# Kernel tuning notes

Measured on AMD Instinct MI355X. Metric: run time of the kernel, lower is better.

Reference implementation:

```python
import jax, jax.numpy as jnp
import numpy as np

B, S, D, H = 2, 2048, 1024, 16
HD = D // H  # 64


def setup_inputs() -> dict:
    key = jax.random.key(0)
    ks = jax.random.split(key, 12)
    scale = 1.0 / np.sqrt(D)
    inp = {
        "input_query": jax.random.normal(ks[0], (B, S, D), jnp.float32),
        "input_key": jax.random.normal(ks[1], (B, S, D), jnp.float32),
        "input_value": jax.random.normal(ks[2], (B, S, D), jnp.float32),
        "mask": jax.random.randint(ks[3], (B, 1, S), 0, 2, jnp.int32),
        # torch nn.Linear params: y = x @ W.T + b, W shape (out, in)
        "wq": jax.random.uniform(ks[4], (D, D), jnp.float32, -scale, scale),
        "bq": jax.random.uniform(ks[5], (D,), jnp.float32, -scale, scale),
        "wk": jax.random.uniform(ks[6], (D, D), jnp.float32, -scale, scale),
        "bk": jax.random.uniform(ks[7], (D,), jnp.float32, -scale, scale),
        "wv": jax.random.uniform(ks[8], (D, D), jnp.float32, -scale, scale),
        "bv": jax.random.uniform(ks[9], (D,), jnp.float32, -scale, scale),
        "wo": jax.random.uniform(ks[10], (D, D), jnp.float32, -scale, scale),
        "bo": jax.random.uniform(ks[11], (D,), jnp.float32, -scale, scale),
    }
    return inp


def _split_heads(x):
    # (B, S, D) -> (B, H, S, HD)
    return x.reshape(B, S, H, HD).transpose(0, 2, 1, 3)


def reference(input_query, input_key, input_value, mask, wq, bq, wk, bk, wv, bv, wo, bo):
    q = _split_heads(input_query @ wq.T + bq)
    k = _split_heads(input_key @ wk.T + bk)
    v = _split_heads(input_value @ wv.T + bv)

    # scaled dot-product attention (materializes [B,H,S,S] as the original does)
    scores = jnp.einsum("bhqd,bhkd->bhqk", q, k) / np.sqrt(HD).astype(np.float32)
    # mask: (B, 1, S) -> unsqueeze(1) -> (B, 1, 1, S); fill -1e9 where mask == 0
    m = mask[:, None, :, :]
    scores = jnp.where(m == 0, jnp.float32(-1e9), scores)
    p_attn = jax.nn.softmax(scores, axis=-1)  # dropout is identity (rate 0 / eval)

    out = jnp.einsum("bhqk,bhkd->bhqd", p_attn, v)
    out = out.transpose(0, 2, 1, 3).reshape(B, S, D)
    return out @ wo.T + bo
```

## Files before the change

kernel.cpp:

```cpp
#include <hip/hip_runtime.h>
#include <math.h>

#define BB 2
#define SS 2048
#define DD 1024
#define HH 16
#define HD 64

typedef short short8 __attribute__((ext_vector_type(8)));
typedef float floatx4 __attribute__((ext_vector_type(4)));
typedef float floatx16 __attribute__((ext_vector_type(16)));
typedef unsigned int uintx2 __attribute__((ext_vector_type(2)));

__device__ inline ushort f2bf_rne(float x) {
    union { float f; unsigned u; } v; v.f = x;
    unsigned r = v.u + 0x7FFFu + ((v.u >> 16) & 1u);
    return (ushort)(r >> 16);
}
__device__ inline float bf2f(ushort h) {
    union { unsigned u; float f; } v; v.u = ((unsigned)h) << 16;
    return v.f;
}
__device__ inline unsigned cvt_pk_bf16(float lo, float hi) {
    unsigned r;
    asm("v_cvt_pk_bf16_f32 %0, %1, %2" : "=v"(r) : "v"(lo), "v"(hi));
    return r;
}
__device__ inline short8 mk_pf(uintx2 x, uintx2 y) {
    union { unsigned u[4]; short8 s; } t;
    t.u[0] = x[0]; t.u[1] = y[0]; t.u[2] = x[1]; t.u[3] = y[1];
    return t.s;
}

__global__ __launch_bounds__(256)
void convert_bf16(const float* __restrict__ xq, const float* __restrict__ xk,
                  const float* __restrict__ xv,
                  const float* __restrict__ wq, const float* __restrict__ wk,
                  const float* __restrict__ wv, const float* __restrict__ wo,
                  ushort* __restrict__ Xq, ushort* __restrict__ Xk,
                  ushort* __restrict__ Xv,
                  ushort* __restrict__ Wq, ushort* __restrict__ Wk,
                  ushort* __restrict__ Wv, ushort* __restrict__ Wo)
{
    const int z = blockIdx.z;
    const size_t i = ((size_t)blockIdx.x * 256 + threadIdx.x) * 8;

    const float* src;
    ushort* dst;
    size_t off;
    if (z < 3) {
        src = (z == 0) ? xq : (z == 1) ? xk : xv;
        dst = (z == 0) ? Xq : (z == 1) ? Xk : Xv;
        off = i;
    } else {
        const int seg = (int)(i >> 20);
        off = i & ((1u << 20) - 1);
        src = (seg == 0) ? wq : (seg == 1) ? wk : (seg == 2) ? wv : wo;
        dst = (seg == 0) ? Wq : (seg == 1) ? Wk : (seg == 2) ? Wv : Wo;
    }
    float x[8];
    *(float4*)&x[0] = *(const float4*)(src + off);
    *(float4*)&x[4] = *(const float4*)(src + off + 4);
    short8 h8;
#pragma unroll
    for (int j = 0; j < 8; ++j) h8[j] = (short)f2bf_rne(x[j]);
    *(short8*)&dst[off] = h8;
}

#define LDK 40

__global__ __launch_bounds__(256, 3)
void qkv_gemm(const ushort* __restrict__ Xq, const ushort* __restrict__ Xk,
              const ushort* __restrict__ Xv,
              const ushort* __restrict__ Wq, const ushort* __restrict__ Wk,
              const ushort* __restrict__ Wv,
              const float* __restrict__ bq, const float* __restrict__ bk,
              const float* __restrict__ bv, const int* __restrict__ mask,
              ushort* __restrict__ Qo, ushort* __restrict__ Ko,
              ushort* __restrict__ Vo, float qscale)
{
    __shared__ ushort Alds[128][LDK];
    __shared__ ushort Blds[128][LDK];

    const int z   = blockIdx.z;
    const int tid = threadIdx.x;

    const ushort* X    = (z == 0) ? Xq : (z == 1) ? Xk : Xv;
    const ushort* W    = (z == 0) ? Wq : (z == 1) ? Wk : Wv;
    const float*  bias = (z == 0) ? bq : (z == 1) ? bk : bv;
    const float   osc  = (z == 0) ? qscale : 1.0f;

    const int lane = tid & 63;
    const int wave = tid >> 6;
    const int wr = wave >> 1;
    const int wc = wave & 1;
    const int lt = lane & 15;
    const int lq = lane >> 4;
    const int m0 = blockIdx.y * 128;
    const int n0 = blockIdx.x * 128;

    floatx4 acc[4][4];
#pragma unroll
    for (int mi = 0; mi < 4; ++mi)
#pragma unroll
        for (int ni = 0; ni < 4; ++ni) acc[mi][ni] = (floatx4)0.0f;

    const int srow = tid >> 1;
    const int sks  = (tid & 1) << 4;
    const size_t xrow = (size_t)(m0 + srow) * DD;
    const size_t wrow = (size_t)(n0 + srow) * DD;

    for (int k0 = 0; k0 < DD; k0 += 32) {
        const short8 a0 = *(const short8*)(X + xrow + k0 + sks);
        const short8 a1 = *(const short8*)(X + xrow + k0 + sks + 8);
        const short8 b0 = *(const short8*)(W + wrow + k0 + sks);
        const short8 b1 = *(const short8*)(W + wrow + k0 + sks + 8);

        __syncthreads();
        *(short8*)&Alds[srow][sks]     = a0;
        *(short8*)&Alds[srow][sks + 8] = a1;
        *(short8*)&Blds[srow][sks]     = b0;
        *(short8*)&Blds[srow][sks + 8] = b1;
        __syncthreads();

        short8 af[4], bf_[4];
#pragma unroll
        for (int mi = 0; mi < 4; ++mi)
            af[mi] = *(const short8*)&Alds[wr * 64 + mi * 16 + lt][lq * 8];
#pragma unroll
        for (int ni = 0; ni < 4; ++ni)
            bf_[ni] = *(const short8*)&Blds[wc * 64 + ni * 16 + lt][lq * 8];

#pragma unroll
        for (int mi = 0; mi < 4; ++mi)
#pragma unroll
            for (int ni = 0; ni < 4; ++ni)
                acc[mi][ni] = __builtin_amdgcn_mfma_f32_16x16x32_bf16(af[mi], bf_[ni], acc[mi][ni], 0, 0, 0);
    }

    float bbv[4];
#pragma unroll
    for (int ni = 0; ni < 4; ++ni) bbv[ni] = bias[n0 + wc * 64 + ni * 16 + lt];

    if (z <= 1) {
        ushort* C = z ? Ko : Qo;
#pragma unroll
        for (int mi = 0; mi < 4; ++mi)
#pragma unroll
            for (int ni = 0; ni < 4; ++ni) {
                const int n = n0 + wc * 64 + ni * 16 + lt;
                const int h = n >> 6;
#pragma unroll
                for (int r = 0; r < 4; ++r) {
                    const int m = m0 + wr * 64 + mi * 16 + lq * 4 + r;
                    const int b = m >> 11;
                    const int s = m & (SS - 1);
                    C[(size_t)((b * HH + h) * SS + s) * HD + (n & 63)] =
                        f2bf_rne((acc[mi][ni][r] + bbv[ni]) * osc);
                }
            }
    } else {
#pragma unroll
        for (int mi = 0; mi < 4; ++mi) {
            const int mb  = m0 + wr * 64 + mi * 16 + lq * 4;
            const int bb_ = mb >> 11;
            const int s   = mb & (SS - 1);
            const int4 mm = *(const int4*)(mask + bb_ * SS + s);
            const float mf0 = (float)mm.x, mf1 = (float)mm.y;
            const float mf2 = (float)mm.z, mf3 = (float)mm.w;
#pragma unroll
            for (int ni = 0; ni < 4; ++ni) {
                const int n = n0 + wc * 64 + ni * 16 + lt;
                const int h = n >> 6;
                ushort4 pack;
                pack.x = f2bf_rne((acc[mi][ni][0] + bbv[ni]) * mf0);
                pack.y = f2bf_rne((acc[mi][ni][1] + bbv[ni]) * mf1);
                pack.z = f2bf_rne((acc[mi][ni][2] + bbv[ni]) * mf2);
                pack.w = f2bf_rne((acc[mi][ni][3] + bbv[ni]) * mf3);
                *(ushort4*)&Vo[(size_t)((bb_ * HH + h) * HD + (n & 63)) * SS + s] = pack;
            }
        }
    }
}

#define ATQ 128
#define LDV 68

__global__ __launch_bounds__(256, 2)
void attn_mfma(const ushort* __restrict__ Qb, const ushort* __restrict__ Kb,
               const ushort* __restrict__ Vt, const int* __restrict__ mask,
               ushort* __restrict__ Ob)
{
    __shared__ __align__(16) ushort Klds[2][64][LDV];
    __shared__ __align__(16) ushort Vlds[2][64][LDV];
    __shared__ __align__(16) ushort Mlds[SS];

    const int tid  = threadIdx.x;
    const int lane = tid & 63;
    const int wave = tid >> 6;
    const int ll   = lane & 31;
    const int hi   = lane >> 5;

    const int bid    = blockIdx.x;
    const int xcd    = bid & 7;
    const int slot   = bid >> 3;
    const int bhloc  = slot >> 4;
    const int qi     = slot & 15;
    const int bh     = xcd * 4 + bhloc;
    const int b      = bh >> 4;
    const int q0     = qi * ATQ;

    const size_t sbase = (size_t)bh * SS * HD;
    const size_t vbase = (size_t)bh * HD * SS;

    {
        const int4 m0 = *(const int4*)(mask + b * SS + tid * 8);
        const int4 m1 = *(const int4*)(mask + b * SS + tid * 8 + 4);
        short8 mv;
        mv[0] = m0.x ? (short)0x3F80 : (short)0;
        mv[1] = m0.y ? (short)0x3F80 : (short)0;
        mv[2] = m0.z ? (short)0x3F80 : (short)0;
        mv[3] = m0.w ? (short)0x3F80 : (short)0;
        mv[4] = m1.x ? (short)0x3F80 : (short)0;
        mv[5] = m1.y ? (short)0x3F80 : (short)0;
        mv[6] = m1.z ? (short)0x3F80 : (short)0;
        mv[7] = m1.w ? (short)0x3F80 : (short)0;
        *(short8*)&Mlds[tid * 8] = mv;
    }

    short8 qf[4];
    const size_t qrow = sbase + (size_t)(q0 + wave * 32 + ll) * HD;
#pragma unroll
    for (int dc = 0; dc < 4; ++dc)
        qf[dc] = *(const short8*)(Qb + qrow + dc * 16 + hi * 8);

    floatx16 oacc[2];
    oacc[0] = (floatx16)0.0f;
    oacc[1] = (floatx16)0.0f;
    floatx16 lacc = (floatx16)0.0f;

    const int srow = tid >> 2;
    const int sp8  = (tid & 3) << 4;

    short8 kr0, kr1, vr0, vr1;

    {
        const size_t koff = sbase + (size_t)srow * HD + sp8;
        kr0 = *(const short8*)(Kb + koff);
        kr1 = *(const short8*)(Kb + koff + 8);
        const size_t voff = vbase + (size_t)srow * SS + sp8;
        vr0 = *(const short8*)(Vt + voff);
        vr1 = *(const short8*)(Vt + voff + 8);
        *(short8*)&Klds[0][srow][sp8]     = kr0;
        *(short8*)&Klds[0][srow][sp8 + 8] = kr1;
        *(short8*)&Vlds[0][srow][sp8]     = vr0;
        *(short8*)&Vlds[0][srow][sp8 + 8] = vr1;
    }

    const int NT = SS / 64;
    for (int kt = 0; kt < NT; ++kt) {
        const int cur = kt & 1;
        __syncthreads();

        if (kt + 1 < NT) {
            const int k0n = (kt + 1) * 64;
            const size_t koff = sbase + (size_t)(k0n + srow) * HD + sp8;
            kr0 = *(const short8*)(Kb + koff);
            kr1 = *(const short8*)(Kb + koff + 8);
            const size_t voff = vbase + (size_t)srow * SS + k0n + sp8;
            vr0 = *(const short8*)(Vt + voff);
            vr1 = *(const short8*)(Vt + voff + 8);
        }

#pragma unroll
        for (int sub = 0; sub < 2; ++sub) {
            floatx16 sacc = (floatx16)0.0f;
#pragma unroll
            for (int dc = 0; dc < 4; ++dc) {
                const short8 kf = *(const short8*)&Klds[cur][sub * 32 + ll][dc * 16 + hi * 8];
                sacc = __builtin_amdgcn_mfma_f32_32x32x16_bf16(kf, qf[dc], sacc, 0, 0, 0);
            }

            float p[16];
#pragma unroll
            for (int r = 0; r < 16; ++r) p[r] = exp2f(sacc[r]);

            const unsigned pk_a = cvt_pk_bf16(p[0],  p[1]);
            const unsigned pk_b = cvt_pk_bf16(p[2],  p[3]);
            const unsigned pk_c = cvt_pk_bf16(p[4],  p[5]);
            const unsigned pk_d = cvt_pk_bf16(p[6],  p[7]);
            const unsigned pk_e = cvt_pk_bf16(p[8],  p[9]);
            const unsigned pk_f = cvt_pk_bf16(p[10], p[11]);
            const unsigned pk_g = cvt_pk_bf16(p[12], p[13]);
            const unsigned pk_h = cvt_pk_bf16(p[14], p[15]);
            const uintx2 s1 = __builtin_amdgcn_permlane32_swap(pk_a, pk_c, false, false);
            const uintx2 s2 = __builtin_amdgcn_permlane32_swap(pk_b, pk_d, false, false);
            const uintx2 s3 = __builtin_amdgcn_permlane32_swap(pk_e, pk_g, false, false);
            const uintx2 s4 = __builtin_amdgcn_permlane32_swap(pk_f, pk_h, false, false);
            const short8 pf0 = mk_pf(s1, s2);
            const short8 pf1 = mk_pf(s3, s4);

            const int kbase = kt * 64 + sub * 32;
            const short8 mf0 = *(const short8*)&Mlds[kbase + hi * 8];
            const short8 mf1 = *(const short8*)&Mlds[kbase + 16 + hi * 8];
            lacc = __builtin_amdgcn_mfma_f32_32x32x16_bf16(pf0, mf0, lacc, 0, 0, 0);
            lacc = __builtin_amdgcn_mfma_f32_32x32x16_bf16(pf1, mf1, lacc, 0, 0, 0);

#pragma unroll
            for (int dn = 0; dn < 2; ++dn) {
                const short8 vf0 = *(const short8*)&Vlds[cur][dn * 32 + ll][sub * 32 + hi * 8];
                const short8 vf1 = *(const short8*)&Vlds[cur][dn * 32 + ll][sub * 32 + 16 + hi * 8];
                oacc[dn] = __builtin_amdgcn_mfma_f32_32x32x16_bf16(pf0, vf0, oacc[dn], 0, 0, 0);
                oacc[dn] = __builtin_amdgcn_mfma_f32_32x32x16_bf16(pf1, vf1, oacc[dn], 0, 0, 0);
            }
        }

        if (kt + 1 < NT) {
            const int nxt = cur ^ 1;
            *(short8*)&Klds[nxt][srow][sp8]     = kr0;
            *(short8*)&Klds[nxt][srow][sp8 + 8] = kr1;
            *(short8*)&Vlds[nxt][srow][sp8]     = vr0;
            *(short8*)&Vlds[nxt][srow][sp8 + 8] = vr1;
        }
    }

    const int h = bh & 15;
    float linv[16];
#pragma unroll
    for (int r = 0; r < 16; ++r) linv[r] = 1.0f / lacc[r];
#pragma unroll
    for (int dn = 0; dn < 2; ++dn)
#pragma unroll
        for (int r = 0; r < 16; ++r) {
            const int q = q0 + wave * 32 + (r & 3) + 8 * (r >> 2) + 4 * hi;
            Ob[(size_t)(b * SS + q) * DD + h * HD + dn * 32 + ll] =
                f2bf_rne(oacc[dn][r] * linv[r]);
        }
}

__global__ __launch_bounds__(256, 3)
void o_gemm(const ushort* __restrict__ A, const ushort* __restrict__ B,
            const float* __restrict__ bias, float* __restrict__ out)
{
    __shared__ ushort sA[128][LDK];
    __shared__ ushort sB[64][LDK];

    const int tid  = threadIdx.x;
    const int lane = tid & 63;
    const int wave = tid >> 6;
    const int wr = wave >> 1;
    const int wc = wave & 1;
    const int lt = lane & 15;
    const int lq = lane >> 4;
    const int m0 = blockIdx.y * 128;
    const int n0 = blockIdx.x * 64;

    floatx4 acc[4][2];
#pragma unroll
    for (int mi = 0; mi < 4; ++mi)
#pragma unroll
        for (int ni = 0; ni < 2; ++ni) acc[mi][ni] = (floatx4)0.0f;

    const int arow = tid >> 1, apart = (tid & 1) << 4;
    const int brow = tid >> 2, bpart = (tid & 3) << 3;

    for (int k0 = 0; k0 < DD; k0 += 32) {
        const size_t aoff = (size_t)(m0 + arow) * DD + k0 + apart;
        const size_t boff = (size_t)(n0 + brow) * DD + k0 + bpart;
        const short8 a0 = *(const short8*)(A + aoff);
        const short8 a1 = *(const short8*)(A + aoff + 8);
        const short8 b0 = *(const short8*)(B + boff);

        __syncthreads();
        *(short8*)&sA[arow][apart]     = a0;
        *(short8*)&sA[arow][apart + 8] = a1;
        *(short8*)&sB[brow][bpart]     = b0;
        __syncthreads();

        short8 af[4], bf_[2];
#pragma unroll
        for (int mi = 0; mi < 4; ++mi)
            af[mi] = *(const short8*)&sA[wr * 64 + mi * 16 + lt][lq * 8];
#pragma unroll
        for (int ni = 0; ni < 2; ++ni)
            bf_[ni] = *(const short8*)&sB[wc * 32 + ni * 16 + lt][lq * 8];

#pragma unroll
        for (int mi = 0; mi < 4; ++mi)
#pragma unroll
            for (int ni = 0; ni < 2; ++ni)
                acc[mi][ni] = __builtin_amdgcn_mfma_f32_16x16x32_bf16(af[mi], bf_[ni], acc[mi][ni], 0, 0, 0);
    }

#pragma unroll
    for (int mi = 0; mi < 4; ++mi)
#pragma unroll
        for (int ni = 0; ni < 2; ++ni) {
            const int n = n0 + wc * 32 + ni * 16 + lt;
            const float bb = bias[n];
#pragma unroll
            for (int r = 0; r < 4; ++r) {
                const int m = m0 + wr * 64 + mi * 16 + lq * 4 + r;
                out[(size_t)m * DD + n] = acc[mi][ni][r] + bb;
            }
        }
}

extern "C" void kernel_launch(void* const* d_in, const int* in_sizes, int n_in,
                              void* d_out, int out_size, void* d_ws, size_t ws_size,
                              hipStream_t stream) {
    const float* xq   = (const float*)d_in[0];
    const float* xk   = (const float*)d_in[1];
    const float* xv   = (const float*)d_in[2];
    const int*   mask = (const int*)d_in[3];
    const float* wq   = (const float*)d_in[4];
    const float* bq   = (const float*)d_in[5];
    const float* wk   = (const float*)d_in[6];
    const float* bk   = (const float*)d_in[7];
    const float* wv   = (const float*)d_in[8];
    const float* bv   = (const float*)d_in[9];
    const float* wo   = (const float*)d_in[10];
    const float* bo   = (const float*)d_in[11];
    float* out = (float*)d_out;

    const size_t n = (size_t)BB * SS * DD;
    const size_t w1 = (size_t)DD * DD;

    ushort* Xqb = (ushort*)d_ws;
    ushort* Xkb = Xqb + n;
    ushort* Xvb = Xkb + n;
    ushort* Kb  = Xvb + n;
    ushort* Vt  = Kb + n;
    ushort* Wob = Vt + n;
    ushort* Ob  = Xqb;

    ushort* Qb  = (ushort*)out;
    ushort* Wqb = Qb + n;
    ushort* Wkb = Wqb + w1;
    ushort* Wvb = Wkb + w1;

    const float qscale = 0.125f * 1.44269504088896340736f;

    dim3 gc(2048, 1, 4);
    convert_bf16<<<gc, 256, 0, stream>>>(xq, xk, xv, wq, wk, wv, wo,
                                         Xqb, Xkb, Xvb, Wqb, Wkb, Wvb, Wob);

    dim3 g1(DD / 128, (BB * SS) / 128, 3);
    qkv_gemm<<<g1, 256, 0, stream>>>(Xqb, Xkb, Xvb, Wqb, Wkb, Wvb,
                                     bq, bk, bv, mask, Qb, Kb, Vt, qscale);

    attn_mfma<<<dim3(512), 256, 0, stream>>>(Qb, Kb, Vt, mask, Ob);

    dim3 g2(DD / 64, (BB * SS) / 128);
    o_gemm<<<g2, 256, 0, stream>>>(Ob, Wob, bo, out);
}
```

Measured before the change: 238.4 us.

## Split attention waves over query pairs and key halves, fold mask into K

The mask is now applied by zeroing masked K rows during the K projection. Masked keys then give a score of zero, so exp2 of them is 1. The row-sum denominator subtracts the count of masked keys, which removes the per-tile mask LDS reads and lets the row sum use a constant ones operand. Each attention wave now handles two 32-row query groups over half of each 64-key tile, so every K fragment read from LDS is reused across two query groups. The two key halves are then combined through shared memory at the end. This adds register pressure, an LDS reduction epilogue and extra syncs, and it relies on masked scores without max-subtraction staying numerically safe.

New measurement: 241.0 us. About the same (+1.1%).

```diff
diff --git a/kernel.cpp b/kernel.cpp
--- a/kernel.cpp
+++ b/kernel.cpp
@@ -142,24 +142,7 @@
 #pragma unroll
     for (int ni = 0; ni < 4; ++ni) bbv[ni] = bias[n0 + wc * 64 + ni * 16 + lt];
 
-    if (z <= 1) {
-        ushort* C = z ? Ko : Qo;
-#pragma unroll
-        for (int mi = 0; mi < 4; ++mi)
-#pragma unroll
-            for (int ni = 0; ni < 4; ++ni) {
-                const int n = n0 + wc * 64 + ni * 16 + lt;
-                const int h = n >> 6;
-#pragma unroll
-                for (int r = 0; r < 4; ++r) {
-                    const int m = m0 + wr * 64 + mi * 16 + lq * 4 + r;
-                    const int b = m >> 11;
-                    const int s = m & (SS - 1);
-                    C[(size_t)((b * HH + h) * SS + s) * HD + (n & 63)] =
-                        f2bf_rne((acc[mi][ni][r] + bbv[ni]) * osc);
-                }
-            }
-    } else {
+    if (z == 2) {
 #pragma unroll
         for (int mi = 0; mi < 4; ++mi) {
             const int mb  = m0 + wr * 64 + mi * 16 + lq * 4;
@@ -180,6 +163,30 @@
                 *(ushort4*)&Vo[(size_t)((bb_ * HH + h) * HD + (n & 63)) * SS + s] = pack;
             }
         }
+    } else {
+        ushort* C = z ? Ko : Qo;
+#pragma unroll
+        for (int mi = 0; mi < 4; ++mi) {
+            const int mb  = m0 + wr * 64 + mi * 16 + lq * 4;
+            const int bb_ = mb >> 11;
+            const int s   = mb & (SS - 1);
+            float mf[4] = {1.0f, 1.0f, 1.0f, 1.0f};
+            if (z == 1) {
+                const int4 mm = *(const int4*)(mask + bb_ * SS + s);
+                mf[0] = (float)mm.x; mf[1] = (float)mm.y;
+                mf[2] = (float)mm.z; mf[3] = (float)mm.w;
+            }
+#pragma unroll
+            for (int ni = 0; ni < 4; ++ni) {
+                const int n = n0 + wc * 64 + ni * 16 + lt;
+                const int h = n >> 6;
+#pragma unroll
+                for (int r = 0; r < 4; ++r) {
+                    C[(size_t)((bb_ * HH + h) * SS + (s + r)) * HD + (n & 63)] =
+                        f2bf_rne((acc[mi][ni][r] + bbv[ni]) * osc * mf[r]);
+                }
+            }
+        }
     }
 }
 
@@ -193,13 +200,17 @@
 {
     __shared__ __align__(16) ushort Klds[2][64][LDV];
     __shared__ __align__(16) ushort Vlds[2][64][LDV];
-    __shared__ __align__(16) ushort Mlds[SS];
+    __shared__ float CmbO[2][2][16][64];
+    __shared__ float CmbL[2][16][64];
+    __shared__ int   Wsum[4];
 
     const int tid  = threadIdx.x;
     const int lane = tid & 63;
     const int wave = tid >> 6;
     const int ll   = lane & 31;
     const int hi   = lane >> 5;
+    const int qh   = wave & 1;
+    const int ks   = wave >> 1;
 
     const int bid    = blockIdx.x;
     const int xcd    = bid & 7;
@@ -214,30 +225,35 @@
     const size_t vbase = (size_t)bh * HD * SS;
 
     {
-        const int4 m0 = *(const int4*)(mask + b * SS + tid * 8);
-        const int4 m1 = *(const int4*)(mask + b * SS + tid * 8 + 4);
-        short8 mv;
-        mv[0] = m0.x ? (short)0x3F80 : (short)0;
-        mv[1] = m0.y ? (short)0x3F80 : (short)0;
-        mv[2] = m0.z ? (short)0x3F80 : (short)0;
-        mv[3] = m0.w ? (short)0x3F80 : (short)0;
-        mv[4] = m1.x ? (short)0x3F80 : (short)0;
-        mv[5] = m1.y ? (short)0x3F80 : (short)0;
-        mv[6] = m1.z ? (short)0x3F80 : (short)0;
-        mv[7] = m1.w ? (short)0x3F80 : (short)0;
-        *(short8*)&Mlds[tid * 8] = mv;
-    }
-
-    short8 qf[4];
-    const size_t qrow = sbase + (size_t)(q0 + wave * 32 + ll) * HD;
-#pragma unroll
-    for (int dc = 0; dc < 4; ++dc)
-        qf[dc] = *(const short8*)(Qb + qrow + dc * 16 + hi * 8);
-
-    floatx16 oacc[2];
-    oacc[0] = (floatx16)0.0f;
-    oacc[1] = (floatx16)0.0f;
-    floatx16 lacc = (floatx16)0.0f;
+        const int4 ma = *(const int4*)(mask + b * SS + tid * 8);
+        const int4 mb = *(const int4*)(mask + b * SS + tid * 8 + 4);
+        int s = ma.x + ma.y + ma.z + ma.w + mb.x + mb.y + mb.z + mb.w;
+#pragma unroll
+        for (int w = 32; w >= 1; w >>= 1) s += __shfl_xor(s, w);
+        if (lane == 0) Wsum[wave] = s;
+    }
+
+    short8 ones;
+#pragma unroll
+    for (int j = 0; j < 8; ++j) ones[j] = (short)0x3F80;
+
+    short8 qf[2][4];
+#pragma unroll
+    for (int g = 0; g < 2; ++g) {
+        const size_t qrow = sbase + (size_t)(q0 + qh * 64 + g * 32 + ll) * HD;
+#pragma unroll
+        for (int dc = 0; dc < 4; ++dc)
+            qf[g][dc] = *(const short8*)(Qb + qrow + dc * 16 + hi * 8);
+    }
+
+    floatx16 oacc[2][2];
+    floatx16 lacc[2];
+#pragma unroll
+    for (int g = 0; g < 2; ++g) {
+        oacc[g][0] = (floatx16)0.0f;
+        oacc[g][1] = (floatx16)0.0f;
+        lacc[g]    = (floatx16)0.0f;
+    }
 
     const int srow = tid >> 2;
     const int sp8  = (tid & 3) << 4;
@@ -272,14 +288,18 @@
             vr1 = *(const short8*)(Vt + voff + 8);
         }
 
-#pragma unroll
-        for (int sub = 0; sub < 2; ++sub) {
+        short8 kf[4];
+#pragma unroll
+        for (int dc = 0; dc < 4; ++dc)
+            kf[dc] = *(const short8*)&Klds[cur][ks * 32 + ll][dc * 16 + hi * 8];
+
+        short8 pf[2][2];
+#pragma unroll
+        for (int g = 0; g < 2; ++g) {
             floatx16 sacc = (floatx16)0.0f;
 #pragma unroll
-            for (int dc = 0; dc < 4; ++dc) {
-                const short8 kf = *(const short8*)&Klds[cur][sub * 32 + ll][dc * 16 + hi * 8];
-                sacc = __builtin_amdgcn_mfma_f32_32x32x16_bf16(kf, qf[dc], sacc, 0, 0, 0);
-            }
+            for (int dc = 0; dc < 4; ++dc)
+                sacc = __builtin_amdgcn_mfma_f32_32x32x16_bf16(kf[dc], qf[g][dc], sacc, 0, 0, 0);
 
             float p[16];
 #pragma unroll
@@ -297,21 +317,24 @@
             const uintx2 s2 = __builtin_amdgcn_permlane32_swap(pk_b, pk_d, false, false);
             const uintx2 s3 = __builtin_amdgcn_permlane32_swap(pk_e, pk_g, false, false);
             const uintx2 s4 = __builtin_amdgcn_permlane32_swap(pk_f, pk_h, false, false);
-            const short8 pf0 = mk_pf(s1, s2);
-            const short8 pf1 = mk_pf(s3, s4);
-
-            const int kbase = kt * 64 + sub * 32;
-            const short8 mf0 = *(const short8*)&Mlds[kbase + hi * 8];
-            const short8 mf1 = *(const short8*)&Mlds[kbase + 16 + hi * 8];
-            lacc = __builtin_amdgcn_mfma_f32_32x32x16_bf16(pf0, mf0, lacc, 0, 0, 0);
-            lacc = __builtin_amdgcn_mfma_f32_32x32x16_bf16(pf1, mf1, lacc, 0, 0, 0);
-
-#pragma unroll
-            for (int dn = 0; dn < 2; ++dn) {
-                const short8 vf0 = *(const short8*)&Vlds[cur][dn * 32 + ll][sub * 32 + hi * 8];
-                const short8 vf1 = *(const short8*)&Vlds[cur][dn * 32 + ll][sub * 32 + 16 + hi * 8];
-                oacc[dn] = __builtin_amdgcn_mfma_f32_32x32x16_bf16(pf0, vf0, oacc[dn], 0, 0, 0);
-                oacc[dn] = __builtin_amdgcn_mfma_f32_32x32x16_bf16(pf1, vf1, oacc[dn], 0, 0, 0);
+            pf[g][0] = mk_pf(s1, s2);
+            pf[g][1] = mk_pf(s3, s4);
+        }
+
+#pragma unroll
+        for (int g = 0; g < 2; ++g) {
+            lacc[g] = __builtin_amdgcn_mfma_f32_32x32x16_bf16(pf[g][0], ones, lacc[g], 0, 0, 0);
+            lacc[g] = __builtin_amdgcn_mfma_f32_32x32x16_bf16(pf[g][1], ones, lacc[g], 0, 0, 0);
+        }
+
+#pragma unroll
+        for (int dn = 0; dn < 2; ++dn) {
+            const short8 vf0 = *(const short8*)&Vlds[cur][dn * 32 + ll][ks * 32 + hi * 8];
+            const short8 vf1 = *(const short8*)&Vlds[cur][dn * 32 + ll][ks * 32 + 16 + hi * 8];
+#pragma unroll
+            for (int g = 0; g < 2; ++g) {
+                oacc[g][dn] = __builtin_amdgcn_mfma_f32_32x32x16_bf16(pf[g][0], vf0, oacc[g][dn], 0, 0, 0);
+                oacc[g][dn] = __builtin_amdgcn_mfma_f32_32x32x16_bf16(pf[g][1], vf1, oacc[g][dn], 0, 0, 0);
             }
         }
 
@@ -324,18 +347,50 @@
         }
     }
 
-    const int h = bh & 15;
-    float linv[16];
-#pragma unroll
-    for (int r = 0; r < 16; ++r) linv[r] = 1.0f / lacc[r];
-#pragma unroll
-    for (int dn = 0; dn < 2; ++dn)
-#pragma unroll
-        for (int r = 0; r < 16; ++r) {
-            const int q = q0 + wave * 32 + (r & 3) + 8 * (r >> 2) + 4 * hi;
-            Ob[(size_t)(b * SS + q) * DD + h * HD + dn * 32 + ll] =
-                f2bf_rne(oacc[dn][r] * linv[r]);
-        }
+#pragma unroll
+    for (int g = 0; g < 2; ++g) {
+        __syncthreads();
+        if (wave >= 2) {
+#pragma unroll
+            for (int dn = 0; dn < 2; ++dn)
+#pragma unroll
+                for (int r = 0; r < 16; ++r)
+                    CmbO[wave - 2][dn][r][lane] = oacc[g][dn][r];
+#pragma unroll
+            for (int r = 0; r < 16; ++r)
+                CmbL[wave - 2][r][lane] = lacc[g][r];
+        }
+        __syncthreads();
+        if (wave < 2) {
+#pragma unroll
+            for (int dn = 0; dn < 2; ++dn)
+#pragma unroll
+                for (int r = 0; r < 16; ++r)
+                    oacc[g][dn][r] += CmbO[wave][dn][r][lane];
+#pragma unroll
+            for (int r = 0; r < 16; ++r)
+                lacc[g][r] += CmbL[wave][r][lane];
+        }
+    }
+
+    if (wave < 2) {
+        const int h = bh & 15;
+        const float nmf = (float)(SS - (Wsum[0] + Wsum[1] + Wsum[2] + Wsum[3]));
+#pragma unroll
+        for (int g = 0; g < 2; ++g) {
+            float linv[16];
+#pragma unroll
+            for (int r = 0; r < 16; ++r) linv[r] = 1.0f / (lacc[g][r] - nmf);
+#pragma unroll
+            for (int dn = 0; dn < 2; ++dn)
+#pragma unroll
+                for (int r = 0; r < 16; ++r) {
+                    const int q = q0 + qh * 64 + g * 32 + (r & 3) + 8 * (r >> 2) + 4 * hi;
+                    Ob[(size_t)(b * SS + q) * DD + h * HD + dn * 32 + ll] =
+                        f2bf_rne(oacc[g][dn][r] * linv[r]);
+                }
+        }
+    }
 }
 
 __global__ __launch_bounds__(256, 3)
```
